# Kernel tuning notes

Measured on AMD Instinct MI355X. Metric: run time of the kernel, lower is better.

The kernel has to match this reference:

```python
import jax, jax.numpy as jnp
import numpy as np
import math

B, NG, LS, E = 2, 8, 512, 1024
NH = 16
HD = E // NH
EPS = 1e-6


def rms_norm(x, w):
    xf = x.astype(jnp.float32)
    n = xf * jax.lax.rsqrt(jnp.mean(xf * xf, axis=-1, keepdims=True) + EPS)
    return n.astype(x.dtype) * w


def rotate(x):
    # pairs (a,b) -> (-b, a), matching view(...,-1,2).flip(-1); x[...,0]*=-1
    x2 = x.reshape(*x.shape[:-1], HD // 2, 2)
    out = jnp.stack([-x2[..., 1], x2[..., 0]], axis=-1)
    return out.reshape(x.shape)


def setup_inputs() -> dict:
    key = jax.random.key(0)
    k1, k2, k3 = jax.random.split(key, 3)
    x = jax.random.normal(k1, (B, NG, LS, E), dtype=jnp.float32)
    W_qkv = jax.random.normal(k2, (E, 3 * E), dtype=jnp.float32) * (1.0 / math.sqrt(E))
    ln_w = jnp.ones((E,), dtype=jnp.float32)
    W_proj = jax.random.normal(k3, (E, E), dtype=jnp.float32) * (1.0 / math.sqrt(E))
    return {"x": x, "W_qkv": W_qkv, "ln_w": ln_w, "W_proj": W_proj}


def reference(x, W_qkv, ln_w, W_proj):
    b, ng, ls, _ = x.shape
    qkv = jnp.einsum('bgsc,ce->bgse', x, W_qkv)  # fused QKV projection
    q, k, v = jnp.split(qkv, 3, axis=-1)
    # QK RMSNorm over full embedding dim (before head split)
    q = rms_norm(q, ln_w)
    k = rms_norm(k, ln_w)
    # [B, ng, nh, ls, hd]
    q = q.reshape(b, ng, ls, NH, HD).swapaxes(2, 3)
    k = k.reshape(b, ng, ls, NH, HD).swapaxes(2, 3)
    v = v.reshape(b, ng, ls, NH, HD).swapaxes(2, 3)
    # RoPE (repo's variant: angles duplicated across halves, adjacent-pair rotate)
    pos = 10000.0 ** ((-2.0 * jnp.arange(0, HD, 2, dtype=jnp.float32) - 1.0) / HD)
    token_seq = jnp.arange(ls, dtype=jnp.float32)[:, None] * pos[None, :]  # [ls, hd/2]
    rot = jnp.concatenate([token_seq, token_seq], axis=-1)  # [ls, hd]
    cos, sin = jnp.cos(rot), jnp.sin(rot)
    q = q * cos + rotate(q) * sin
    k = k * cos + rotate(k) * sin
    # causal attention, scale = 1/sqrt(head_dim) (muP=False)
    scale = 1.0 / math.sqrt(HD)
    scores = jnp.einsum('bgnqd,bgnkd->bgnqk', q, k) * scale
    causal = jnp.tril(jnp.ones((ls, ls), dtype=bool))
    scores = jnp.where(causal, scores, jnp.finfo(scores.dtype).min)
    att = jax.nn.softmax(scores, axis=-1)
    y = jnp.einsum('bgnqk,bgnkd->bgnqd', att, v)
    y = y.swapaxes(2, 3).reshape(b, ng, ls, E)
    y = jnp.einsum('bgse,ef->bgsf', y, W_proj)
    return y
```

## Files before the change

kernel.cpp:

```cpp
#include <hip/hip_runtime.h>

typedef unsigned short u16;
typedef unsigned int   u32;
typedef __attribute__((ext_vector_type(8))) short bf16x8;
typedef __attribute__((ext_vector_type(4))) float f32x4;

#define MFMA16(a,b,c) __builtin_amdgcn_mfma_f32_16x16x32_bf16((a),(b),(c),0,0,0)
#define GLD16(gp, lp) __builtin_amdgcn_global_load_lds((const __attribute__((address_space(1))) u32*)(gp), (__attribute__((address_space(3))) u32*)(lp), 16, 0, 0)

#define B_   2
#define NG_  8
#define LS_  512
#define E_   1024
#define NH_  16
#define HD_  64
#define NTOK 8192

__device__ __forceinline__ u16 f2bu(float f){
  u32 u = __builtin_bit_cast(u32, f);
  u32 r = u + 0x7FFFu + ((u >> 16) & 1u);
  return (u16)(r >> 16);
}
__device__ __forceinline__ float b2f(u16 h){
  u32 u = ((u32)h) << 16;
  return __builtin_bit_cast(float, u);
}
__device__ __forceinline__ u32 pk2(float lo, float hi){
  u32 r; asm("v_cvt_pk_bf16_f32 %0, %1, %2" : "=v"(r) : "v"(lo), "v"(hi)); return r;
}

__global__ __launch_bounds__(256) void k_prep(const float* __restrict__ x, u16* __restrict__ xb,
                                              const float* __restrict__ Wqkv, u16* __restrict__ wqkvT,
                                              const float* __restrict__ Wproj, u16* __restrict__ wprojT,
                                              float* __restrict__ ct, float* __restrict__ st){
  int b = blockIdx.x;
  if (b < 8192){
    int i = b * 256 + threadIdx.x;
    float4 v = ((const float4*)x)[i];
    ((ushort4*)xb)[i] = make_ushort4(f2bu(v.x), f2bu(v.y), f2bu(v.z), f2bu(v.w));
    return;
  }
  if (b < 12288){
    const float* W; u16* WT; int Nd, bl;
    if (b < 11264){ W = Wqkv;  WT = wqkvT;  Nd = 3072; bl = b - 8192;  }
    else          { W = Wproj; WT = wprojT; Nd = 1024; bl = b - 11264; }
    int nbx = Nd >> 5;
    int bx = bl % nbx, by = bl / nbx;
    __shared__ float tile[32][33];
    int tx = threadIdx.x & 31, ty = threadIdx.x >> 5;
    int c0 = bx * 32, r0 = by * 32;
    #pragma unroll
    for (int i = 0; i < 4; i++)
      tile[ty + i*8][tx] = W[(size_t)(r0 + ty + i*8) * Nd + c0 + tx];
    __syncthreads();
    #pragma unroll
    for (int i = 0; i < 4; i++)
      WT[(size_t)(c0 + ty + i*8) * 1024 + r0 + tx] = f2bu(tile[tx][ty + i*8]);
    return;
  }
  {
    int i = (b - 12288) * 256 + threadIdx.x;
    int s = i >> 6, d = i & 63, j = d & 31;
    float freq = powf(10000.f, -(4.f * (float)j + 1.f) / 64.f);
    float th = (float)s * freq;
    ct[i] = cosf(th);
    st[i] = sinf(th);
  }
}

template <typename OutT, bool FUSE_VT>
__global__ __launch_bounds__(256, 2) void k_gemm_bt(const u16* __restrict__ A, const u16* __restrict__ Bt,
                                                    OutT* __restrict__ C, u16* __restrict__ vt,
                                                    int M, int N, int K){
  int nbn = N >> 7;
  int cpx = gridDim.x >> 3;
  int xcd = blockIdx.x & 7;
  int ii  = blockIdx.x >> 3;
  int rpx = cpx / nbn;
  int tm, tn;
  if ((nbn % 6) == 0 && (rpx & 3) == 0){
    int st = ii / 24, wi = ii % 24;
    int srn = rpx >> 2;
    int sr = st % srn, sc = st / srn;
    tm = xcd * rpx + sr * 4 + (wi / 6);
    tn = sc * 6 + (wi % 6);
  } else {
    int bid = xcd * cpx + ii;
    tm = bid / nbn; tn = bid % nbn;
  }
  int tid = threadIdx.x;
  int w = tid >> 6, l = tid & 63;
  int lr = l & 15, lg = l >> 4;
  int wm = (w >> 1) * 64, wn = (w & 1) * 64;

  __shared__ u16 smem[2][2][128 * 64];

  const u16* Ab = A  + (size_t)(tm * 128) * K;
  const u16* Bb = Bt + (size_t)(tn * 128) * K;
  int NT = K >> 6;

  int srow0 = tid >> 3, ssl = tid & 7;
  auto stage = [&](int t, int s){
    int k0 = t << 6;
    #pragma unroll
    for (int q = 0; q < 4; q++){
      int row = q * 32 + srow0;
      int sc2 = (ssl ^ (row & 7)) << 3;
      GLD16(Ab + (size_t)row * K + k0 + sc2, &smem[s][0][q * 2048 + tid * 8]);
    }
    #pragma unroll
    for (int q = 0; q < 4; q++){
      int row = q * 32 + srow0;
      int sc2 = (ssl ^ (row & 7)) << 3;
      GLD16(Bb + (size_t)row * K + k0 + sc2, &smem[s][1][q * 2048 + tid * 8]);
    }
  };

  f32x4 acc[4][4] = {};

  stage(0, 0);
  stage(1, 1);
  asm volatile("s_waitcnt vmcnt(8)" ::: "memory");
  asm volatile("s_barrier" ::: "memory");

  for (int t = 0; t < NT; t++){
    int s = t & 1;
    const u16* As = smem[s][0];
    const u16* Bs = smem[s][1];
    bf16x8 bfr[4][2], afr[2][2];
    #pragma unroll
    for (int j = 0; j < 4; j++){
      int rb = wn + j * 16 + lr;
      #pragma unroll
      for (int kk = 0; kk < 2; kk++)
        bfr[j][kk] = *(const bf16x8*)&Bs[rb * 64 + ((kk * 32 + lg * 8) ^ ((rb & 7) << 3))];
    }
    #pragma unroll
    for (int i = 0; i < 2; i++){
      int ra = wm + i * 16 + lr;
      #pragma unroll
      for (int kk = 0; kk < 2; kk++)
        afr[i][kk] = *(const bf16x8*)&As[ra * 64 + ((kk * 32 + lg * 8) ^ ((ra & 7) << 3))];
    }
    __builtin_amdgcn_s_setprio(1);
    #pragma unroll
    for (int i = 0; i < 2; i++)
      #pragma unroll
      for (int j = 0; j < 4; j++){
        acc[i][j] = MFMA16(afr[i][0], bfr[j][0], acc[i][j]);
        acc[i][j] = MFMA16(afr[i][1], bfr[j][1], acc[i][j]);
      }
    __builtin_amdgcn_s_setprio(0);
    asm volatile("s_barrier" ::: "memory");
    #pragma unroll
    for (int i = 0; i < 2; i++){
      int ra = wm + (i + 2) * 16 + lr;
      #pragma unroll
      for (int kk = 0; kk < 2; kk++)
        afr[i][kk] = *(const bf16x8*)&As[ra * 64 + ((kk * 32 + lg * 8) ^ ((ra & 7) << 3))];
    }
    __builtin_amdgcn_s_setprio(1);
    #pragma unroll
    for (int i = 0; i < 2; i++)
      #pragma unroll
      for (int j = 0; j < 4; j++){
        acc[i + 2][j] = MFMA16(afr[i][0], bfr[j][0], acc[i + 2][j]);
        acc[i + 2][j] = MFMA16(afr[i][1], bfr[j][1], acc[i + 2][j]);
      }
    __builtin_amdgcn_s_setprio(0);
    asm volatile("s_barrier" ::: "memory");
    if (t + 2 < NT){
      stage(t + 2, s);
      asm volatile("s_waitcnt vmcnt(8)" ::: "memory");
      asm volatile("s_barrier" ::: "memory");
    } else if (t + 2 == NT){
      asm volatile("s_waitcnt vmcnt(0)" ::: "memory");
      asm volatile("s_barrier" ::: "memory");
    }
  }

  if constexpr (FUSE_VT){
    if (tn >= 16){
      int h  = (tn - 16) * 2 + (wn >> 6);
      int bg = tm >> 2;
      u16* vbase = vt + (size_t)(bg * 16 + h) * HD_ * LS_;
      #pragma unroll
      for (int i = 0; i < 4; i++){
        int s0 = (tm & 3) * 128 + wm + i * 16 + lg * 4;
        #pragma unroll
        for (int j = 0; j < 4; j++){
          int d = j * 16 + lr;
          ushort4 pk = make_ushort4(f2bu(acc[i][j][0]), f2bu(acc[i][j][1]),
                                    f2bu(acc[i][j][2]), f2bu(acc[i][j][3]));
          *(ushort4*)&vbase[(size_t)d * LS_ + s0] = pk;
        }
      }
      return;
    }
  }

  #pragma unroll
  for (int i = 0; i < 4; i++)
    #pragma unroll
    for (int j = 0; j < 4; j++)
      #pragma unroll
      for (int r = 0; r < 4; r++){
        int row = tm * 128 + wm + i * 16 + lg * 4 + r;
        int col = tn * 128 + wn + j * 16 + lr;
        float v = acc[i][j][r];
        if constexpr (sizeof(OutT) == 2) C[(size_t)row * N + col] = f2bu(v);
        else                             C[(size_t)row * N + col] = v;
      }
}

__global__ __launch_bounds__(256) void k_norm_rope(const u16* __restrict__ qkv, const float* __restrict__ lnw,
                                                   const float* __restrict__ ct, const float* __restrict__ st,
                                                   u16* __restrict__ qh, u16* __restrict__ kh){
  int tok = blockIdx.x;
  int t = threadIdx.x;
  int s = tok & (LS_ - 1);
  int bg = tok >> 9;
  const u16* row = qkv + (size_t)tok * 3072;
  int e0 = t * 4;

  ushort4 q4 = *(const ushort4*)&row[e0];
  ushort4 k4 = *(const ushort4*)&row[1024 + e0];
  float qf[4] = {b2f(q4.x), b2f(q4.y), b2f(q4.z), b2f(q4.w)};
  float kf[4] = {b2f(k4.x), b2f(k4.y), b2f(k4.z), b2f(k4.w)};

  float qss = 0.f, kss = 0.f;
  #pragma unroll
  for (int j = 0; j < 4; j++){ qss += qf[j]*qf[j]; kss += kf[j]*kf[j]; }
  #pragma unroll
  for (int o = 32; o; o >>= 1){ qss += __shfl_down(qss, o); kss += __shfl_down(kss, o); }
  __shared__ float redq[4], redk[4];
  if ((t & 63) == 0){ redq[t >> 6] = qss; redk[t >> 6] = kss; }
  __syncthreads();
  float qsum = redq[0] + redq[1] + redq[2] + redq[3];
  float ksum = redk[0] + redk[1] + redk[2] + redk[3];
  float qr = rsqrtf(qsum * (1.f / 1024.f) + 1e-6f);
  float kr = rsqrtf(ksum * (1.f / 1024.f) + 1e-6f);

  float qn[4], kn[4];
  #pragma unroll
  for (int j = 0; j < 4; j++){
    float wv = lnw[e0 + j];
    qn[j] = qf[j] * qr * wv;
    kn[j] = kf[j] * kr * wv;
  }
  int d0 = e0 & 63, h = e0 >> 6;
  const float* cr = ct + s * 64 + d0;
  const float* sr = st + s * 64 + d0;
  float qo[4], ko[4];
  #pragma unroll
  for (int p = 0; p < 4; p += 2){
    float c0 = cr[p], s0 = sr[p], c1 = cr[p+1], s1 = sr[p+1];
    qo[p]   = qn[p]   * c0 - qn[p+1] * s0;
    qo[p+1] = qn[p+1] * c1 + qn[p]   * s1;
    ko[p]   = kn[p]   * c0 - kn[p+1] * s0;
    ko[p+1] = kn[p+1] * c1 + kn[p]   * s1;
  }
  size_t oidx = (((size_t)bg * NH_ + h) * LS_ + s) * HD_ + d0;
  *(ushort4*)&qh[oidx] = make_ushort4(f2bu(qo[0]*0.125f), f2bu(qo[1]*0.125f), f2bu(qo[2]*0.125f), f2bu(qo[3]*0.125f));
  *(ushort4*)&kh[oidx] = make_ushort4(f2bu(ko[0]), f2bu(ko[1]), f2bu(ko[2]), f2bu(ko[3]));
}

__global__ __launch_bounds__(64) void k_attn(const u16* __restrict__ qh, const u16* __restrict__ kh,
                                             const u16* __restrict__ vt, u16* __restrict__ ytok){
  int bid = blockIdx.x;
  int head = bid & 255;
  int j = 15 - (bid >> 8);
  int l = threadIdx.x & 63;
  int lr = l & 15, lg = l >> 4;
  int q0 = j * 32;
  int ntw = (j >> 1) + 1;

  const u16* Qp = qh + (size_t)head * LS_ * HD_;
  const u16* Kp = kh + (size_t)head * LS_ * HD_;
  const u16* Vp = vt + (size_t)head * HD_ * LS_;
  int bg = head >> 4, h = head & 15;
  u16* Yb = ytok + (size_t)bg * LS_ * E_ + h * HD_;

  bf16x8 aq[2][2];
  #pragma unroll
  for (int mi = 0; mi < 2; mi++)
    #pragma unroll
    for (int kk = 0; kk < 2; kk++)
      aq[mi][kk] = *(const bf16x8*)&Qp[(q0 + mi*16 + lr) * 64 + kk * 32 + lg * 8];

  __shared__ u16 Pw[32 * 72];

  f32x4 o[2][4] = {};
  float mrun[2] = {-1e30f, -1e30f}, lrun[2] = {0.f, 0.f};

  for (int tkv = 0; tkv < ntw; tkv++){
    int kv0 = tkv * 64;
    f32x4 sa[2][4] = {};
    __builtin_amdgcn_s_setprio(1);
    #pragma unroll
    for (int nk = 0; nk < 4; nk++){
      bf16x8 k0 = *(const bf16x8*)&Kp[(kv0 + nk*16 + lr) * 64 + lg * 8];
      bf16x8 k1 = *(const bf16x8*)&Kp[(kv0 + nk*16 + lr) * 64 + 32 + lg * 8];
      #pragma unroll
      for (int mi = 0; mi < 2; mi++){
        sa[mi][nk] = MFMA16(k0, aq[mi][0], sa[mi][nk]);
        sa[mi][nk] = MFMA16(k1, aq[mi][1], sa[mi][nk]);
      }
    }
    __builtin_amdgcn_s_setprio(0);
    if (kv0 + 63 > q0){
      #pragma unroll
      for (int mi = 0; mi < 2; mi++){
        int qg = q0 + mi*16 + lr;
        #pragma unroll
        for (int nk = 0; nk < 4; nk++)
          #pragma unroll
          for (int r = 0; r < 4; r++){
            int kg = kv0 + nk*16 + lg*4 + r;
            if (kg > qg) sa[mi][nk][r] = -1e30f;
          }
      }
    }
    float pmax[2];
    #pragma unroll
    for (int mi = 0; mi < 2; mi++){
      float pm = sa[mi][0][0];
      #pragma unroll
      for (int nk = 0; nk < 4; nk++)
        #pragma unroll
        for (int r = 0; r < 4; r++) pm = fmaxf(pm, sa[mi][nk][r]);
      pm = fmaxf(pm, __shfl_xor(pm, 16));
      pm = fmaxf(pm, __shfl_xor(pm, 32));
      pmax[mi] = pm;
    }
    float dm = fmaxf(pmax[0] - mrun[0], pmax[1] - mrun[1]);
    if (!__all(dm <= 8.f)){
      float alpha[2];
      #pragma unroll
      for (int mi = 0; mi < 2; mi++){
        float mnew = fmaxf(mrun[mi], pmax[mi]);
        alpha[mi] = __expf(mrun[mi] - mnew);
        mrun[mi] = mnew;
        lrun[mi] *= alpha[mi];
      }
      #pragma unroll
      for (int r = 0; r < 4; r++){
        float a0 = __shfl(alpha[0], lg * 4 + r);
        float a1 = __shfl(alpha[1], lg * 4 + r);
        #pragma unroll
        for (int nd = 0; nd < 4; nd++){ o[0][nd][r] *= a0; o[1][nd][r] *= a1; }
      }
    }
    #pragma unroll
    for (int mi = 0; mi < 2; mi++){
      float psum = 0.f;
      #pragma unroll
      for (int nk = 0; nk < 4; nk++)
        #pragma unroll
        for (int r = 0; r < 4; r++){
          float pv = __expf(sa[mi][nk][r] - mrun[mi]);
          sa[mi][nk][r] = pv;
          psum += pv;
        }
      psum += __shfl_xor(psum, 16);
      psum += __shfl_xor(psum, 32);
      lrun[mi] += psum;
    }
    #pragma unroll
    for (int mi = 0; mi < 2; mi++)
      #pragma unroll
      for (int nk = 0; nk < 4; nk++){
        *(u32*)&Pw[(mi*16 + lr) * 72 + nk * 16 + lg * 4]     = pk2(sa[mi][nk][0], sa[mi][nk][1]);
        *(u32*)&Pw[(mi*16 + lr) * 72 + nk * 16 + lg * 4 + 2] = pk2(sa[mi][nk][2], sa[mi][nk][3]);
      }
    bf16x8 pa[2][2];
    #pragma unroll
    for (int mi = 0; mi < 2; mi++){
      pa[mi][0] = *(const bf16x8*)&Pw[(mi*16 + lr) * 72 + lg * 8];
      pa[mi][1] = *(const bf16x8*)&Pw[(mi*16 + lr) * 72 + 32 + lg * 8];
    }
    __builtin_amdgcn_s_setprio(1);
    #pragma unroll
    for (int nd = 0; nd < 4; nd++){
      bf16x8 bv0 = *(const bf16x8*)&Vp[(nd*16 + lr) * 512 + kv0 + lg * 8];
      bf16x8 bv1 = *(const bf16x8*)&Vp[(nd*16 + lr) * 512 + kv0 + 32 + lg * 8];
      #pragma unroll
      for (int mi = 0; mi < 2; mi++){
        o[mi][nd] = MFMA16(pa[mi][0], bv0, o[mi][nd]);
        o[mi][nd] = MFMA16(pa[mi][1], bv1, o[mi][nd]);
      }
    }
    __builtin_amdgcn_s_setprio(0);
  }

  #pragma unroll
  for (int mi = 0; mi < 2; mi++){
    float linv = 1.f / lrun[mi];
    #pragma unroll
    for (int r = 0; r < 4; r++){
      float ir = __shfl(linv, lg * 4 + r);
      int qg = q0 + mi*16 + lg * 4 + r;
      #pragma unroll
      for (int nd = 0; nd < 4; nd++)
        Yb[(size_t)qg * E_ + nd * 16 + lr] = f2bu(o[mi][nd][r] * ir);
    }
  }
}

extern "C" void kernel_launch(void* const* d_in, const int* in_sizes, int n_in,
                              void* d_out, int out_size, void* d_ws, size_t ws_size,
                              hipStream_t stream){
  const float* x     = (const float*)d_in[0];
  const float* Wqkv  = (const float*)d_in[1];
  const float* lnw   = (const float*)d_in[2];
  const float* Wproj = (const float*)d_in[3];
  float* out = (float*)d_out;

  u16* p = (u16*)d_ws;
  u16* xb     = p; p += (size_t)NTOK * E_;
  u16* wqkvT  = p; p += (size_t)3 * E_ * E_;
  u16* wprojT = p; p += (size_t)E_ * E_;
  u16* qkv    = p; p += (size_t)NTOK * 3 * E_;
  u16* qhp    = p; p += (size_t)NTOK * E_;
  u16* khp    = p; p += (size_t)NTOK * E_;
  u16* vtp    = p; p += (size_t)NTOK * E_;
  float* ct = (float*)p;
  float* st = ct + LS_ * HD_;

  k_prep<<<12416, 256, 0, stream>>>(x, xb, Wqkv, wqkvT, Wproj, wprojT, ct, st);
  k_gemm_bt<u16, true><<<64 * 24, 256, 0, stream>>>(xb, wqkvT, qkv, vtp, NTOK, 3 * E_, E_);
  k_norm_rope<<<NTOK, 256, 0, stream>>>(qkv, lnw, ct, st, qhp, khp);
  k_attn<<<4096, 64, 0, stream>>>(qhp, khp, vtp, xb);
  k_gemm_bt<float, false><<<64 * 8, 256, 0, stream>>>(xb, wprojT, out, nullptr, NTOK, E_, E_);
}
```

Baseline: 150.8 us.

## Enlarge GEMM tile to 128x256 with 8 waves and triple-buffered LDS pipeline

The bf16 GEMM kernel moves from 128x128 tiles with 4 waves to 128x256 tiles with 8 waves (512 threads, one block per CU). LDS grows to three buffers, and global-to-LDS staging is split into two phases interleaved with the two k-halves of the MFMA work. This aims to raise data reuse per loaded byte and hide load latency better. The cost is lower occupancy, fewer blocks (768 and 256), and possible tail imbalance on the small projection GEMM.

After: 160.9 us. 1.07x slower.

```diff
diff --git a/kernel.cpp b/kernel.cpp
--- a/kernel.cpp
+++ b/kernel.cpp
@@ -69,10 +69,10 @@
 }
 
 template <typename OutT, bool FUSE_VT>
-__global__ __launch_bounds__(256, 2) void k_gemm_bt(const u16* __restrict__ A, const u16* __restrict__ Bt,
+__global__ __launch_bounds__(512, 1) void k_gemm_bt(const u16* __restrict__ A, const u16* __restrict__ Bt,
                                                     OutT* __restrict__ C, u16* __restrict__ vt,
                                                     int M, int N, int K){
-  int nbn = N >> 7;
+  int nbn = N >> 8;
   int cpx = gridDim.x >> 3;
   int xcd = blockIdx.x & 7;
   int ii  = blockIdx.x >> 3;
@@ -91,107 +91,118 @@
   int tid = threadIdx.x;
   int w = tid >> 6, l = tid & 63;
   int lr = l & 15, lg = l >> 4;
-  int wm = (w >> 1) * 64, wn = (w & 1) * 64;
-
-  __shared__ u16 smem[2][2][128 * 64];
+  int wr = w >> 2, wc = w & 3;
+
+  __shared__ u16 sA[3 * 128 * 64];
+  __shared__ u16 sB[3 * 256 * 64];
 
   const u16* Ab = A  + (size_t)(tm * 128) * K;
-  const u16* Bb = Bt + (size_t)(tn * 128) * K;
+  const u16* Bb = Bt + (size_t)(tn * 256) * K;
   int NT = K >> 6;
 
-  int srow0 = tid >> 3, ssl = tid & 7;
-  auto stage = [&](int t, int s){
+  int rowt = tid >> 3, slot = tid & 7;
+  auto stage_ph0 = [&](int t, int b){
     int k0 = t << 6;
     #pragma unroll
-    for (int q = 0; q < 4; q++){
-      int row = q * 32 + srow0;
-      int sc2 = (ssl ^ (row & 7)) << 3;
-      GLD16(Ab + (size_t)row * K + k0 + sc2, &smem[s][0][q * 2048 + tid * 8]);
-    }
-    #pragma unroll
-    for (int q = 0; q < 4; q++){
-      int row = q * 32 + srow0;
-      int sc2 = (ssl ^ (row & 7)) << 3;
-      GLD16(Bb + (size_t)row * K + k0 + sc2, &smem[s][1][q * 2048 + tid * 8]);
+    for (int q = 0; q < 2; q++){
+      int row = q * 64 + rowt;
+      int sc2 = (slot ^ (row & 7)) << 3;
+      GLD16(Ab + (size_t)row * K + k0 + sc2, &sA[b * 8192 + q * 4096 + tid * 8]);
+    }
+    {
+      int row = rowt;
+      int sc2 = (slot ^ (row & 7)) << 3;
+      GLD16(Bb + (size_t)row * K + k0 + sc2, &sB[b * 16384 + tid * 8]);
     }
   };
+  auto stage_ph1 = [&](int t, int b){
+    int k0 = t << 6;
+    #pragma unroll
+    for (int q = 1; q < 4; q++){
+      int row = q * 64 + rowt;
+      int sc2 = (slot ^ (row & 7)) << 3;
+      GLD16(Bb + (size_t)row * K + k0 + sc2, &sB[b * 16384 + q * 4096 + tid * 8]);
+    }
+  };
 
   f32x4 acc[4][4] = {};
 
-  stage(0, 0);
-  stage(1, 1);
-  asm volatile("s_waitcnt vmcnt(8)" ::: "memory");
+  stage_ph0(0, 0); stage_ph1(0, 0);
+  stage_ph0(1, 1); stage_ph1(1, 1);
+  asm volatile("s_waitcnt vmcnt(6)" ::: "memory");
   asm volatile("s_barrier" ::: "memory");
 
+  int bi = 0;
   for (int t = 0; t < NT; t++){
-    int s = t & 1;
-    const u16* As = smem[s][0];
-    const u16* Bs = smem[s][1];
-    bf16x8 bfr[4][2], afr[2][2];
-    #pragma unroll
-    for (int j = 0; j < 4; j++){
-      int rb = wn + j * 16 + lr;
-      #pragma unroll
-      for (int kk = 0; kk < 2; kk++)
-        bfr[j][kk] = *(const bf16x8*)&Bs[rb * 64 + ((kk * 32 + lg * 8) ^ ((rb & 7) << 3))];
-    }
-    #pragma unroll
-    for (int i = 0; i < 2; i++){
-      int ra = wm + i * 16 + lr;
-      #pragma unroll
-      for (int kk = 0; kk < 2; kk++)
-        afr[i][kk] = *(const bf16x8*)&As[ra * 64 + ((kk * 32 + lg * 8) ^ ((ra & 7) << 3))];
-    }
+    const u16* As = &sA[bi * 8192];
+    const u16* Bs = &sB[bi * 16384];
+    int b2 = bi + 2; if (b2 >= 3) b2 -= 3;
+    bool do_stage = (t + 2 < NT);
+
+    bf16x8 af[4], bf[4];
+    #pragma unroll
+    for (int m = 0; m < 4; m++){
+      int ra = wr * 64 + m * 16 + lr;
+      af[m] = *(const bf16x8*)&As[ra * 64 + ((lg * 8) ^ ((ra & 7) << 3))];
+    }
+    #pragma unroll
+    for (int n = 0; n < 4; n++){
+      int rb = wc * 64 + n * 16 + lr;
+      bf[n] = *(const bf16x8*)&Bs[rb * 64 + ((lg * 8) ^ ((rb & 7) << 3))];
+    }
+    if (do_stage) stage_ph0(t + 2, b2);
+    asm volatile("s_barrier" ::: "memory");
+    asm volatile("s_waitcnt lgkmcnt(0)" ::: "memory");
     __builtin_amdgcn_s_setprio(1);
     #pragma unroll
-    for (int i = 0; i < 2; i++)
-      #pragma unroll
-      for (int j = 0; j < 4; j++){
-        acc[i][j] = MFMA16(afr[i][0], bfr[j][0], acc[i][j]);
-        acc[i][j] = MFMA16(afr[i][1], bfr[j][1], acc[i][j]);
-      }
+    for (int m = 0; m < 4; m++)
+      #pragma unroll
+      for (int n = 0; n < 4; n++)
+        acc[m][n] = MFMA16(af[m], bf[n], acc[m][n]);
     __builtin_amdgcn_s_setprio(0);
     asm volatile("s_barrier" ::: "memory");
-    #pragma unroll
-    for (int i = 0; i < 2; i++){
-      int ra = wm + (i + 2) * 16 + lr;
-      #pragma unroll
-      for (int kk = 0; kk < 2; kk++)
-        afr[i][kk] = *(const bf16x8*)&As[ra * 64 + ((kk * 32 + lg * 8) ^ ((ra & 7) << 3))];
-    }
+
+    #pragma unroll
+    for (int m = 0; m < 4; m++){
+      int ra = wr * 64 + m * 16 + lr;
+      af[m] = *(const bf16x8*)&As[ra * 64 + ((32 + lg * 8) ^ ((ra & 7) << 3))];
+    }
+    #pragma unroll
+    for (int n = 0; n < 4; n++){
+      int rb = wc * 64 + n * 16 + lr;
+      bf[n] = *(const bf16x8*)&Bs[rb * 64 + ((32 + lg * 8) ^ ((rb & 7) << 3))];
+    }
+    if (do_stage) stage_ph1(t + 2, b2);
+    asm volatile("s_barrier" ::: "memory");
+    asm volatile("s_waitcnt lgkmcnt(0)" ::: "memory");
     __builtin_amdgcn_s_setprio(1);
     #pragma unroll
-    for (int i = 0; i < 2; i++)
-      #pragma unroll
-      for (int j = 0; j < 4; j++){
-        acc[i + 2][j] = MFMA16(afr[i][0], bfr[j][0], acc[i + 2][j]);
-        acc[i + 2][j] = MFMA16(afr[i][1], bfr[j][1], acc[i + 2][j]);
-      }
+    for (int m = 0; m < 4; m++)
+      #pragma unroll
+      for (int n = 0; n < 4; n++)
+        acc[m][n] = MFMA16(af[m], bf[n], acc[m][n]);
     __builtin_amdgcn_s_setprio(0);
+
+    if (t + 2 < NT)       asm volatile("s_waitcnt vmcnt(6)" ::: "memory");
+    else if (t + 1 < NT)  asm volatile("s_waitcnt vmcnt(0)" ::: "memory");
     asm volatile("s_barrier" ::: "memory");
-    if (t + 2 < NT){
-      stage(t + 2, s);
-      asm volatile("s_waitcnt vmcnt(8)" ::: "memory");
-      asm volatile("s_barrier" ::: "memory");
-    } else if (t + 2 == NT){
-      asm volatile("s_waitcnt vmcnt(0)" ::: "memory");
-      asm volatile("s_barrier" ::: "memory");
-    }
+
+    bi = bi + 1; if (bi == 3) bi = 0;
   }
 
   if constexpr (FUSE_VT){
-    if (tn >= 16){
-      int h  = (tn - 16) * 2 + (wn >> 6);
+    if (tn >= 8){
+      int h  = (tn - 8) * 4 + wc;
       int bg = tm >> 2;
       u16* vbase = vt + (size_t)(bg * 16 + h) * HD_ * LS_;
       #pragma unroll
-      for (int i = 0; i < 4; i++){
-        int s0 = (tm & 3) * 128 + wm + i * 16 + lg * 4;
+      for (int m = 0; m < 4; m++){
+        int s0 = (tm & 3) * 128 + wr * 64 + m * 16 + lg * 4;
         #pragma unroll
-        for (int j = 0; j < 4; j++){
-          int d = j * 16 + lr;
-          ushort4 pk = make_ushort4(f2bu(acc[i][j][0]), f2bu(acc[i][j][1]),
-                                    f2bu(acc[i][j][2]), f2bu(acc[i][j][3]));
+        for (int n = 0; n < 4; n++){
+          int d = n * 16 + lr;
+          ushort4 pk = make_ushort4(f2bu(acc[m][n][0]), f2bu(acc[m][n][1]),
+                                    f2bu(acc[m][n][2]), f2bu(acc[m][n][3]));
           *(ushort4*)&vbase[(size_t)d * LS_ + s0] = pk;
         }
       }
@@ -200,14 +211,14 @@
   }
 
   #pragma unroll
-  for (int i = 0; i < 4; i++)
-    #pragma unroll
-    for (int j = 0; j < 4; j++)
+  for (int m = 0; m < 4; m++)
+    #pragma unroll
+    for (int n = 0; n < 4; n++)
       #pragma unroll
       for (int r = 0; r < 4; r++){
-        int row = tm * 128 + wm + i * 16 + lg * 4 + r;
-        int col = tn * 128 + wn + j * 16 + lr;
-        float v = acc[i][j][r];
+        int row = tm * 128 + wr * 64 + m * 16 + lg * 4 + r;
+        int col = tn * 256 + wc * 64 + n * 16 + lr;
+        float v = acc[m][n][r];
         if constexpr (sizeof(OutT) == 2) C[(size_t)row * N + col] = f2bu(v);
         else                             C[(size_t)row * N + col] = v;
       }
@@ -428,8 +439,8 @@
   float* st = ct + LS_ * HD_;
 
   k_prep<<<12416, 256, 0, stream>>>(x, xb, Wqkv, wqkvT, Wproj, wprojT, ct, st);
-  k_gemm_bt<u16, true><<<64 * 24, 256, 0, stream>>>(xb, wqkvT, qkv, vtp, NTOK, 3 * E_, E_);
+  k_gemm_bt<u16, true><<<768, 512, 0, stream>>>(xb, wqkvT, qkv, vtp, NTOK, 3 * E_, E_);
   k_norm_rope<<<NTOK, 256, 0, stream>>>(qkv, lnw, ct, st, qhp, khp);
   k_attn<<<4096, 64, 0, stream>>>(qhp, khp, vtp, xb);
-  k_gemm_bt<float, false><<<64 * 8, 256, 0, stream>>>(xb, wprojT, out, nullptr, NTOK, E_, E_);
-}
+  k_gemm_bt<float, false><<<256, 512, 0, stream>>>(xb, wprojT, out, nullptr, NTOK, E_, E_);
+}
```
